# Performance work log

Measured on AMD Instinct MI355X. Metric: run time of the kernel, lower is better.

## Reference

```python
import jax, jax.numpy as jnp
import numpy as np

N = 6144
D = 128
TAU = 0.1
ADJ_P = 0.005  # edge density


def _l2_normalize(x, eps=1e-12):
    # matches torch F.normalize: x / max(||x||, eps)
    n = jnp.sqrt(jnp.sum(x * x, axis=-1, keepdims=True))
    return x / jnp.maximum(n, eps)


def setup_inputs() -> dict:
    key = jax.random.key(0)
    ks = jax.random.split(key, 8)
    embF = jax.random.normal(ks[0], (N, D), jnp.float32)
    embM = jax.random.normal(ks[1], (N, D), jnp.float32)
    embP = jax.random.normal(ks[2], (N, D), jnp.float32)
    FM_adj = (jax.random.uniform(ks[3], (N, N)) < ADJ_P).astype(jnp.float32)
    FP_adj = (jax.random.uniform(ks[4], (N, N)) < ADJ_P).astype(jnp.float32)
    W1 = jax.random.normal(ks[5], (2 * D, D), jnp.float32) * (1.0 / np.sqrt(2 * D))
    b1 = jnp.zeros((D,), jnp.float32)
    W2 = jax.random.normal(ks[6], (D, 2), jnp.float32) * (1.0 / np.sqrt(D))
    b2 = jnp.zeros((2,), jnp.float32)
    return {"embF": embF, "embM": embM, "embP": embP,
            "FM_adj": FM_adj, "FP_adj": FP_adj,
            "W1": W1, "b1": b1, "W2": W2, "b2": b2}


def reference(embF, embM, embP, FM_adj, FP_adj, W1, b1, W2, b2):
    # attention-weighted neighbor aggregation
    FM_repr = (FM_adj @ embM) / jnp.maximum(FM_adj.sum(1, keepdims=True), 1.0)
    FP_repr = (FP_adj @ embP) / jnp.maximum(FP_adj.sum(1, keepdims=True), 1.0)
    # stack(dim=1).view(N,-1) == concat along feature dim
    feat = jnp.concatenate([FM_repr, FP_repr], axis=1)            # [N, 2D]
    h = jnp.maximum(feat @ W1 + b1, 0.0)                           # ReLU (dropout inactive in eval)
    weights = jax.nn.softmax(h @ W2 + b2, axis=-1)                 # [N, 2]

    Fn = _l2_normalize(embF)
    Mn = _l2_normalize(embM)
    Pn = _l2_normalize(embP)

    FM_sim = jnp.exp((Fn @ Mn.T) / TAU)                            # [N, Nm]
    FP_sim = jnp.exp((Fn @ Pn.T) / TAU)                            # [N, Np]

    FM_pos = jnp.sum(FM_sim * FM_adj, axis=1)
    FP_pos = jnp.sum(FP_sim * FP_adj, axis=1)
    FM_neg = jnp.sum(FM_sim, axis=1) - FM_pos
    FP_neg = jnp.sum(FP_sim, axis=1) - FP_pos

    w0, w1w = weights[:, 0], weights[:, 1]
    wp = w0 * FM_pos + w1w * FP_pos
    wn = w0 * FM_neg + w1w * FP_neg

    nei_count = jnp.maximum(FM_adj.sum(1) + FP_adj.sum(1), 1.0)
    ratio = wp / (wp + wn) / nei_count
    ratio = jnp.maximum(ratio, 1e-10)
    loss = jnp.mean(-jnp.log(ratio))
    return loss, weights
```

## Files before the change

kernel.cpp:

```cpp
#include <hip/hip_runtime.h>
#include <hip/hip_bf16.h>

#define NN 6144
#define DD 128
#define PBL 136
#define INV_TAU 10.0f

typedef __attribute__((ext_vector_type(4))) float f32x4;
typedef __attribute__((ext_vector_type(8))) short s16x8;

__device__ __forceinline__ void ld4_async(const float4* p, float4& d) {
    asm volatile("global_load_dwordx4 %0, %1, off" : "=v"(d) : "v"(p));
}
__device__ __forceinline__ void vm_wait0() {
    asm volatile("s_waitcnt vmcnt(0)" ::: "memory");
}

__global__ void k_normalize(const float* __restrict__ embF,
                            const float* __restrict__ embM,
                            const float* __restrict__ embP,
                            float* __restrict__ Fn,
                            float* __restrict__ rnM, float* __restrict__ rnP,
                            __hip_bfloat16* __restrict__ Fnb,
                            __hip_bfloat16* __restrict__ Mnb,
                            __hip_bfloat16* __restrict__ Pnb) {
    int which = blockIdx.y;
    const float* src = which == 0 ? embF : (which == 1 ? embM : embP);
    __hip_bfloat16* dstb = which == 0 ? Fnb : (which == 1 ? Mnb : Pnb);
    int wave = threadIdx.x >> 6, lane = threadIdx.x & 63;
    int row = blockIdx.x * 4 + wave;
    float2 v = reinterpret_cast<const float2*>(src + (size_t)row * DD)[lane];
    float s = v.x * v.x + v.y * v.y;
#pragma unroll
    for (int m = 1; m <= 32; m <<= 1) s += __shfl_xor(s, m);
    float inv = 1.0f / fmaxf(sqrtf(s), 1e-12f);
    float2 o; o.x = v.x * inv; o.y = v.y * inv;
    if (which == 0)
        reinterpret_cast<float2*>(Fn + (size_t)row * DD)[lane] = o;
    if (lane == 0) {
        if (which == 1) rnM[row] = inv;
        if (which == 2) rnP[row] = inv;
    }
    __hip_bfloat162 ob;
    ob.x = __float2bfloat16(o.x);
    ob.y = __float2bfloat16(o.y);
    reinterpret_cast<__hip_bfloat162*>(dstb + (size_t)row * DD)[lane] = ob;
}

__global__ __launch_bounds__(256) void k_sparse2(
        const float* __restrict__ FM_adj, const float* __restrict__ FP_adj,
        const float* __restrict__ embM, const float* __restrict__ embP,
        const float* __restrict__ Fn,
        const float* __restrict__ rnM, const float* __restrict__ rnP,
        float* __restrict__ feat,
        float* __restrict__ FMpos, float* __restrict__ FPpos,
        float* __restrict__ cntF, float* __restrict__ cntP) {
    __shared__ float FnS[DD];
    __shared__ int lbufT[256][4];
    __shared__ int listS[128];
    __shared__ float reprS[8][DD];
    __shared__ float posS[8];
    __shared__ int wvS[4];
    __shared__ int Ktot[2];
    const int row = blockIdx.x, h = blockIdx.y;
    const float* adj  = h ? FP_adj : FM_adj;
    const float* embX = h ? embP : embM;
    const float* RN   = h ? rnP : rnM;
    const int tid = threadIdx.x, wv = tid >> 6, lane = tid & 63;

    if (tid < 32)
        reinterpret_cast<float4*>(FnS)[tid] =
            reinterpret_cast<const float4*>(Fn + (size_t)row * DD)[tid];

    const float4* rp = reinterpret_cast<const float4*>(adj + (size_t)row * NN);
    float4 v0, v1, v2, v3, v4, v5;
    ld4_async(rp + tid,        v0);
    ld4_async(rp + 256 + tid,  v1);
    ld4_async(rp + 512 + tid,  v2);
    ld4_async(rp + 768 + tid,  v3);
    ld4_async(rp + 1024 + tid, v4);
    ld4_async(rp + 1280 + tid, v5);
    vm_wait0();
    float4 vv[6] = {v0, v1, v2, v3, v4, v5};
    int mycnt = 0;
#pragma unroll
    for (int u = 0; u < 6; ++u) {
        int cb = (u * 256 + tid) * 4;
        if (vv[u].x != 0.f) { if (mycnt < 4) lbufT[tid][mycnt] = cb;     mycnt++; }
        if (vv[u].y != 0.f) { if (mycnt < 4) lbufT[tid][mycnt] = cb + 1; mycnt++; }
        if (vv[u].z != 0.f) { if (mycnt < 4) lbufT[tid][mycnt] = cb + 2; mycnt++; }
        if (vv[u].w != 0.f) { if (mycnt < 4) lbufT[tid][mycnt] = cb + 3; mycnt++; }
    }
    int cnt = mycnt < 4 ? mycnt : 4;
    int x = cnt;
#pragma unroll
    for (int d = 1; d < 64; d <<= 1) {
        int y = __shfl_up(x, d);
        if (lane >= d) x += y;
    }
    int t = mycnt;
#pragma unroll
    for (int msk = 1; msk <= 32; msk <<= 1) t += __shfl_xor(t, msk);
    if (tid == 0) Ktot[1] = 0;
    if (lane == 63) wvS[wv] = x;
    __syncthreads();
    if (lane == 0) atomicAdd(&Ktot[1], t);
    if (tid == 0) {
        int s = 0;
#pragma unroll
        for (int i = 0; i < 4; ++i) { int v = wvS[i]; wvS[i] = s; s += v; }
        Ktot[0] = s < 128 ? s : 128;
    }
    __syncthreads();
    int off = wvS[wv] + (x - cnt);
    for (int i = 0; i < cnt; ++i) {
        int s = off + i;
        if (s < 128) listS[s] = lbufT[tid][i];
    }
    __syncthreads();
    const int K = Ktot[0];
    const float trueK = (float)Ktot[1];

    const int hw = tid >> 5, sl = tid & 31;
    float4 f4 = reinterpret_cast<const float4*>(FnS)[sl];
    float4 racc = {0.f, 0.f, 0.f, 0.f};
    float wsum = 0.f;
    for (int k = hw; k < K; k += 8) {
        int j = listS[k];
        float rn = RN[j];
        float4 e = reinterpret_cast<const float4*>(embX + (size_t)j * DD)[sl];
        racc.x += e.x; racc.y += e.y; racc.z += e.z; racc.w += e.w;
        float d = f4.x * e.x + f4.y * e.y + f4.z * e.z + f4.w * e.w;
#pragma unroll
        for (int msk = 1; msk <= 16; msk <<= 1) d += __shfl_xor(d, msk);
        wsum += __expf(d * rn * INV_TAU);
    }
    reinterpret_cast<float4*>(&reprS[hw][0])[sl] = racc;
    if (sl == 0) posS[hw] = wsum;
    __syncthreads();
    if (tid < DD) {
        float s = 0.f;
#pragma unroll
        for (int i = 0; i < 8; ++i) s += reprS[i][tid];
        feat[(size_t)row * (2 * DD) + h * DD + tid] = s / fmaxf(trueK, 1.0f);
    }
    if (tid == 0) {
        float p = 0.f;
#pragma unroll
        for (int i = 0; i < 8; ++i) p += posS[i];
        (h ? FPpos : FMpos)[row] = p;
        (h ? cntP : cntF)[row] = trueK;
    }
}

__global__ __launch_bounds__(256) void k_dense(
        const __hip_bfloat16* __restrict__ Fnb,
        const __hip_bfloat16* __restrict__ Mnb,
        const __hip_bfloat16* __restrict__ Pnb,
        float* __restrict__ FMtot, float* __restrict__ FPtot) {
    __shared__ __hip_bfloat16 Bs[64][PBL];
    const int half = blockIdx.z;
    const __hip_bfloat16* Bnb = half ? Pnb : Mnb;
    float* TOT = half ? FPtot : FMtot;
    const int tid = threadIdx.x;
    const int w = tid >> 6, lane = tid & 63;
    const int m = lane & 15, q = lane >> 4;
    const int rb = blockIdx.x * 128 + w * 32;
    const int j0 = blockIdx.y * (NN / 16);

    s16x8 a[2][4];
#pragma unroll
    for (int g = 0; g < 2; ++g)
#pragma unroll
        for (int ks = 0; ks < 4; ++ks)
            a[g][ks] = *reinterpret_cast<const s16x8*>(
                Fnb + (size_t)(rb + g * 16 + m) * DD + ks * 32 + q * 8);

    float4 s0, s1, s2, s3;
    auto issue = [&](int jc) {
        const float4* gp = reinterpret_cast<const float4*>(Bnb + (size_t)jc * DD);
        ld4_async(gp + tid,       s0);
        ld4_async(gp + 256 + tid, s1);
        ld4_async(gp + 512 + tid, s2);
        ld4_async(gp + 768 + tid, s3);
    };
    auto stash = [&](int idx, const float4& v) {
        *reinterpret_cast<float4*>(&Bs[idx >> 4][(idx & 15) * 8]) = v;
    };

    issue(j0);
    float tot[2][4] = {{0.f, 0.f, 0.f, 0.f}, {0.f, 0.f, 0.f, 0.f}};
    for (int it = 0; it < 6; ++it) {
        vm_wait0();
        __syncthreads();
        stash(tid, s0);
        stash(256 + tid, s1);
        stash(512 + tid, s2);
        stash(768 + tid, s3);
        __syncthreads();
        if (it + 1 < 6) issue(j0 + (it + 1) * 64);
#pragma unroll
        for (int t = 0; t < 4; ++t) {
            s16x8 b[4];
#pragma unroll
            for (int ks = 0; ks < 4; ++ks)
                b[ks] = *reinterpret_cast<const s16x8*>(
                    &Bs[t * 16 + m][ks * 32 + q * 8]);
#pragma unroll
            for (int g = 0; g < 2; ++g) {
                f32x4 acc = {0.f, 0.f, 0.f, 0.f};
#pragma unroll
                for (int ks = 0; ks < 4; ++ks)
                    acc = __builtin_amdgcn_mfma_f32_16x16x32_bf16(
                        a[g][ks], b[ks], acc, 0, 0, 0);
#pragma unroll
                for (int r = 0; r < 4; ++r)
                    tot[g][r] += __expf(acc[r] * INV_TAU);
            }
        }
    }
#pragma unroll
    for (int msk = 1; msk <= 8; msk <<= 1)
#pragma unroll
        for (int g = 0; g < 2; ++g)
#pragma unroll
            for (int r = 0; r < 4; ++r)
                tot[g][r] += __shfl_xor(tot[g][r], msk);
    if (m == 0)
#pragma unroll
        for (int g = 0; g < 2; ++g)
#pragma unroll
            for (int r = 0; r < 4; ++r)
                atomicAdd(&TOT[rb + g * 16 + q * 4 + r], tot[g][r]);
}

__global__ __launch_bounds__(256) void k_mlp(
        const float* __restrict__ feat,
        const float* __restrict__ W1, const float* __restrict__ b1,
        const float* __restrict__ W2, const float* __restrict__ b2,
        const float* __restrict__ FMpos, const float* __restrict__ FPpos,
        const float* __restrict__ FMtot, const float* __restrict__ FPtot,
        const float* __restrict__ cntF, const float* __restrict__ cntP,
        float* __restrict__ out) {
    __shared__ float featS[4][2 * DD];
    __shared__ float partS[2][4][DD];
    __shared__ float redS[2][4][2];
    __shared__ float lossS[4];
    const int tid = threadIdx.x;
    const int cp = tid >> 7, d = tid & 127;
    const int row0 = blockIdx.x * 4;
    for (int idx = tid; idx < 4 * 2 * DD; idx += 256)
        featS[idx >> 8][idx & 255] = feat[(size_t)row0 * (2 * DD) + idx];
    __syncthreads();
    float bb = (cp == 0) ? b1[d] : 0.f;
    float acc[4];
#pragma unroll
    for (int r = 0; r < 4; ++r) acc[r] = bb;
    const int c0 = cp * 128;
    for (int c = c0; c < c0 + 128; c += 2) {
        float wA = W1[c * DD + d];
        float wB = W1[(c + 1) * DD + d];
#pragma unroll
        for (int r = 0; r < 4; ++r)
            acc[r] = fmaf(featS[r][c + 1], wB, fmaf(featS[r][c], wA, acc[r]));
    }
#pragma unroll
    for (int r = 0; r < 4; ++r) partS[cp][r][d] = acc[r];
    __syncthreads();
    if (tid < 128) {
        const int lane = tid & 63, wv = tid >> 6;
        float w20 = W2[2 * tid], w21 = W2[2 * tid + 1];
        float p0s[4], p1s[4];
#pragma unroll
        for (int r = 0; r < 4; ++r) {
            float hh = fmaxf(partS[0][r][tid] + partS[1][r][tid], 0.f);
            p0s[r] = hh * w20;
            p1s[r] = hh * w21;
        }
#pragma unroll
        for (int r = 0; r < 4; ++r)
#pragma unroll
            for (int msk = 1; msk <= 32; msk <<= 1) {
                p0s[r] += __shfl_xor(p0s[r], msk);
                p1s[r] += __shfl_xor(p1s[r], msk);
            }
        if (lane == 0)
#pragma unroll
            for (int r = 0; r < 4; ++r) {
                redS[wv][r][0] = p0s[r];
                redS[wv][r][1] = p1s[r];
            }
    }
    __syncthreads();
    if (tid < 4) {
        int row = row0 + tid;
        float z0 = redS[0][tid][0] + redS[1][tid][0] + b2[0];
        float z1 = redS[0][tid][1] + redS[1][tid][1] + b2[1];
        float mx = fmaxf(z0, z1);
        float e0 = expf(z0 - mx), e1 = expf(z1 - mx);
        float inv = 1.0f / (e0 + e1);
        float w0 = e0 * inv, w1 = e1 * inv;
        out[1 + row * 2 + 0] = w0;
        out[1 + row * 2 + 1] = w1;
        float wp = w0 * FMpos[row] + w1 * FPpos[row];
        float wn = w0 * (FMtot[row] - FMpos[row]) +
                   w1 * (FPtot[row] - FPpos[row]);
        float nei = fmaxf(cntF[row] + cntP[row], 1.0f);
        float ratio = wp / (wp + wn) / nei;
        ratio = fmaxf(ratio, 1e-10f);
        lossS[tid] = -logf(ratio);
    }
    __syncthreads();
    if (tid == 0) {
        float L = 0.f;
#pragma unroll
        for (int r = 0; r < 4; ++r) L += lossS[r];
        atomicAdd(out, L * (1.0f / NN));
    }
}

extern "C" void kernel_launch(void* const* d_in, const int* in_sizes, int n_in,
                              void* d_out, int out_size, void* d_ws, size_t ws_size,
                              hipStream_t stream) {
    const float* embF   = (const float*)d_in[0];
    const float* embM   = (const float*)d_in[1];
    const float* embP   = (const float*)d_in[2];
    const float* FM_adj = (const float*)d_in[3];
    const float* FP_adj = (const float*)d_in[4];
    const float* W1     = (const float*)d_in[5];
    const float* b1     = (const float*)d_in[6];
    const float* W2     = (const float*)d_in[7];
    const float* b2     = (const float*)d_in[8];
    float* out = (float*)d_out;

    float* ws = (float*)d_ws;
    float* FMtot = ws;
    float* FPtot = FMtot + NN;
    float* FMpos = FPtot + NN;
    float* FPpos = FMpos + NN;
    float* cntF  = FPpos + NN;
    float* cntP  = cntF + NN;
    float* rnM   = cntP + NN;
    float* rnP   = rnM + NN;
    float* feat  = rnP + NN;
    float* Fn    = feat + (size_t)NN * 2 * DD;
    __hip_bfloat16* Fnb = (__hip_bfloat16*)(Fn + (size_t)NN * DD);
    __hip_bfloat16* Mnb = Fnb + (size_t)NN * DD;
    __hip_bfloat16* Pnb = Mnb + (size_t)NN * DD;

    hipMemsetAsync(FMtot, 0, 2 * NN * sizeof(float), stream);
    hipMemsetAsync(d_out, 0, sizeof(float), stream);

    k_normalize<<<dim3(NN / 4, 3), 256, 0, stream>>>(embF, embM, embP,
                                                     Fn, rnM, rnP,
                                                     Fnb, Mnb, Pnb);
    k_sparse2<<<dim3(NN, 2), 256, 0, stream>>>(FM_adj, FP_adj, embM, embP,
                                               Fn, rnM, rnP, feat,
                                               FMpos, FPpos, cntF, cntP);
    k_dense<<<dim3(NN / 128, 16, 2), 256, 0, stream>>>(Fnb, Mnb, Pnb,
                                                       FMtot, FPtot);
    k_mlp<<<dim3(NN / 4), 256, 0, stream>>>(feat, W1, b1, W2, b2,
                                            FMpos, FPpos, FMtot, FPtot,
                                            cntF, cntP, out);
}
```

Measured before the change: 395.0 us.

## Merge sparse and dense kernels into one interleaved launch

Combines the memory-bound sparse adjacency kernel and the compute-bound dense similarity kernel into a single launch. Each group of nine blocks holds eight sparse units and one dense unit, so both kinds of work can share the GPU at the same time. Both bodies use one shared-memory buffer sized for the dense tile. The costs are a larger shared-memory footprint for sparse blocks, which may lower occupancy, and higher register pressure from the merged kernel.

```diff
diff --git a/kernel.cpp b/kernel.cpp
--- a/kernel.cpp
+++ b/kernel.cpp
@@ -47,7 +47,8 @@
     reinterpret_cast<__hip_bfloat162*>(dstb + (size_t)row * DD)[lane] = ob;
 }
 
-__global__ __launch_bounds__(256) void k_sparse2(
+__device__ __forceinline__ void sparse_body(
+        int unit, char* smem,
         const float* __restrict__ FM_adj, const float* __restrict__ FP_adj,
         const float* __restrict__ embM, const float* __restrict__ embP,
         const float* __restrict__ Fn,
@@ -55,14 +56,15 @@
         float* __restrict__ feat,
         float* __restrict__ FMpos, float* __restrict__ FPpos,
         float* __restrict__ cntF, float* __restrict__ cntP) {
-    __shared__ float FnS[DD];
-    __shared__ int lbufT[256][4];
-    __shared__ int listS[128];
-    __shared__ float reprS[8][DD];
-    __shared__ float posS[8];
-    __shared__ int wvS[4];
-    __shared__ int Ktot[2];
-    const int row = blockIdx.x, h = blockIdx.y;
+    float* FnS = (float*)smem;
+    int (*lbufT)[4] = (int(*)[4])(smem + 512);
+    int* listS = (int*)(smem + 512 + 4096);
+    float (*reprS)[DD] = (float(*)[DD])(smem + 512 + 4096 + 512);
+    float* posS = (float*)(smem + 512 + 4096 + 512 + 4096);
+    int* wvS = (int*)(smem + 512 + 4096 + 512 + 4096 + 32);
+    int* Ktot = (int*)(smem + 512 + 4096 + 512 + 4096 + 32 + 16);
+
+    const int row = unit >> 1, h = unit & 1;
     const float* adj  = h ? FP_adj : FM_adj;
     const float* embX = h ? embP : embM;
     const float* RN   = h ? rnP : rnM;
@@ -153,20 +155,21 @@
     }
 }
 
-__global__ __launch_bounds__(256) void k_dense(
+__device__ __forceinline__ void dense_body(
+        int unit, char* smem,
         const __hip_bfloat16* __restrict__ Fnb,
         const __hip_bfloat16* __restrict__ Mnb,
         const __hip_bfloat16* __restrict__ Pnb,
         float* __restrict__ FMtot, float* __restrict__ FPtot) {
-    __shared__ __hip_bfloat16 Bs[64][PBL];
-    const int half = blockIdx.z;
+    __hip_bfloat16 (*Bs)[PBL] = (__hip_bfloat16(*)[PBL])smem;
+    const int bx = unit % 48, by = (unit / 48) % 16, half = unit / 768;
     const __hip_bfloat16* Bnb = half ? Pnb : Mnb;
     float* TOT = half ? FPtot : FMtot;
     const int tid = threadIdx.x;
     const int w = tid >> 6, lane = tid & 63;
     const int m = lane & 15, q = lane >> 4;
-    const int rb = blockIdx.x * 128 + w * 32;
-    const int j0 = blockIdx.y * (NN / 16);
+    const int rb = bx * 128 + w * 32;
+    const int j0 = by * (NN / 16);
 
     s16x8 a[2][4];
 #pragma unroll
@@ -232,6 +235,28 @@
 #pragma unroll
             for (int r = 0; r < 4; ++r)
                 atomicAdd(&TOT[rb + g * 16 + q * 4 + r], tot[g][r]);
+}
+
+__global__ __launch_bounds__(256) void k_main(
+        const float* __restrict__ FM_adj, const float* __restrict__ FP_adj,
+        const float* __restrict__ embM, const float* __restrict__ embP,
+        const float* __restrict__ Fn,
+        const float* __restrict__ rnM, const float* __restrict__ rnP,
+        const __hip_bfloat16* __restrict__ Fnb,
+        const __hip_bfloat16* __restrict__ Mnb,
+        const __hip_bfloat16* __restrict__ Pnb,
+        float* __restrict__ feat,
+        float* __restrict__ FMpos, float* __restrict__ FPpos,
+        float* __restrict__ FMtot, float* __restrict__ FPtot,
+        float* __restrict__ cntF, float* __restrict__ cntP) {
+    __shared__ char smem[64 * PBL * 2];
+    const int b = blockIdx.x;
+    const int u = b / 9, r = b - u * 9;
+    if (r == 8)
+        dense_body(u, smem, Fnb, Mnb, Pnb, FMtot, FPtot);
+    else
+        sparse_body(u * 8 + r, smem, FM_adj, FP_adj, embM, embP,
+                    Fn, rnM, rnP, feat, FMpos, FPpos, cntF, cntP);
 }
 
 __global__ __launch_bounds__(256) void k_mlp(
@@ -354,11 +379,10 @@
     k_normalize<<<dim3(NN / 4, 3), 256, 0, stream>>>(embF, embM, embP,
                                                      Fn, rnM, rnP,
                                                      Fnb, Mnb, Pnb);
-    k_sparse2<<<dim3(NN, 2), 256, 0, stream>>>(FM_adj, FP_adj, embM, embP,
-                                               Fn, rnM, rnP, feat,
-                                               FMpos, FPpos, cntF, cntP);
-    k_dense<<<dim3(NN / 128, 16, 2), 256, 0, stream>>>(Fnb, Mnb, Pnb,
-                                                       FMtot, FPtot);
+    k_main<<<dim3(13824), 256, 0, stream>>>(FM_adj, FP_adj, embM, embP,
+                                            Fn, rnM, rnP, Fnb, Mnb, Pnb,
+                                            feat, FMpos, FPpos, FMtot, FPtot,
+                                            cntF, cntP);
     k_mlp<<<dim3(NN / 4), 256, 0, stream>>>(feat, W1, b1, W2, b2,
                                             FMpos, FPpos, FMtot, FPtot,
                                             cntF, cntP, out);
```

New measurement: 384.2 us. -2.7%, faster.
